# Performance work log

Measured on AMD Instinct MI355X. Metric: run time of the kernel, lower is better.

Reference implementation:

```python
import jax, jax.numpy as jnp
import numpy as np

EMBED = 256; HEADS = 8; LEVELS = 4; POINTS = 4; HID = 1024
HD = EMBED // HEADS
SHAPES = [(100, 100), (50, 50), (25, 25), (13, 13)]
STARTS = [0]
for _h, _w in SHAPES[:-1]:
    STARTS.append(STARTS[-1] + _h * _w)
TOTAL = sum(h * w for h, w in SHAPES)
BS = 2
EPS = 1e-5


def _ln(x, g, b):
    m = x.mean(-1, keepdims=True)
    v = ((x - m) ** 2).mean(-1, keepdims=True)
    return (x - m) / jnp.sqrt(v + EPS) * g + b


def _msda(query, value, ref, norm_wh, params):
    W_value, b_value, W_off, b_off, W_attn, b_attn, W_out, b_out = params
    bs, T, _ = query.shape
    v = (value @ W_value + b_value).reshape(bs, T, HEADS, HD)
    v = jnp.moveaxis(v, 2, 1)  # [bs, H, T, hd]
    off = (query @ W_off + b_off).reshape(bs, T, HEADS, LEVELS, POINTS, 2)
    aw = (query @ W_attn + b_attn).reshape(bs, T, HEADS, LEVELS * POINTS)
    aw = jax.nn.softmax(aw, axis=-1).reshape(bs, T, HEADS, LEVELS, POINTS)
    aw = jnp.moveaxis(aw, 2, 1)  # [bs, H, T, L, P]
    # sampling locations in [0,1] coords: ref + offset / (W_l, H_l)
    loc = ref[:, :, None, :, None, :] + off / norm_wh[None, None, None, :, None, :]
    loc = jnp.moveaxis(loc, 2, 1)  # [bs, H, T, L, P, 2]
    out = jnp.zeros((bs, HEADS, T, HD), query.dtype)
    for l, (Hl, Wl) in enumerate(SHAPES):
        s = STARTS[l]
        v_l = v[:, :, s:s + Hl * Wl]  # [bs, H, HW_l, hd]
        # grid_sample(align_corners=False): pixel = loc * size - 0.5
        x = loc[:, :, :, l, :, 0] * Wl - 0.5  # [bs, H, T, P]
        y = loc[:, :, :, l, :, 1] * Hl - 0.5
        x0 = jnp.floor(x); y0 = jnp.floor(y)
        wx1 = x - x0; wy1 = y - y0
        x0i = x0.astype(jnp.int32); y0i = y0.astype(jnp.int32)

        def samp(xi, yi):
            valid = (xi >= 0) & (xi < Wl) & (yi >= 0) & (yi < Hl)
            idx = jnp.clip(yi, 0, Hl - 1) * Wl + jnp.clip(xi, 0, Wl - 1)
            idx = idx.reshape(bs, HEADS, -1)
            g = jnp.take_along_axis(v_l, idx[..., None], axis=2)
            g = g.reshape(bs, HEADS, T, POINTS, HD)
            return g * valid[..., None].astype(g.dtype)

        bil = ((1 - wy1) * (1 - wx1))[..., None] * samp(x0i, y0i) \
            + ((1 - wy1) * wx1)[..., None] * samp(x0i + 1, y0i) \
            + (wy1 * (1 - wx1))[..., None] * samp(x0i, y0i + 1) \
            + (wy1 * wx1)[..., None] * samp(x0i + 1, y0i + 1)
        out = out + (bil * aw[:, :, :, l, :, None]).sum(axis=3)
    out = jnp.moveaxis(out, 1, 2).reshape(bs, T, EMBED)
    return out @ W_out + b_out


def setup_inputs() -> dict:
    key = jax.random.key(0)
    ks = jax.random.split(key, 16)
    s = 0.02
    f32 = jnp.float32
    return {
        "src": jax.random.normal(ks[0], (BS, TOTAL, EMBED), f32),
        "pos": jax.random.normal(ks[1], (BS, TOTAL, EMBED), f32),
        "reference_points": jax.random.uniform(ks[2], (BS, TOTAL, LEVELS, 2), f32),
        "spatial_shapes": jnp.array(SHAPES, jnp.int32),
        "level_start_index": jnp.array(STARTS, jnp.int32),
        "ln1_g": jnp.ones((EMBED,), f32), "ln1_b": jnp.zeros((EMBED,), f32),
        "ln2_g": jnp.ones((EMBED,), f32), "ln2_b": jnp.zeros((EMBED,), f32),
        "W_value": jax.random.normal(ks[3], (EMBED, EMBED), f32) * s,
        "b_value": jnp.zeros((EMBED,), f32),
        "W_off": jax.random.normal(ks[4], (EMBED, HEADS * LEVELS * POINTS * 2), f32) * s,
        "b_off": jax.random.normal(ks[5], (HEADS * LEVELS * POINTS * 2,), f32) * 0.5,
        "W_attn": jax.random.normal(ks[6], (EMBED, HEADS * LEVELS * POINTS), f32) * s,
        "b_attn": jnp.zeros((HEADS * LEVELS * POINTS,), f32),
        "W_out": jax.random.normal(ks[7], (EMBED, EMBED), f32) * s,
        "b_out": jnp.zeros((EMBED,), f32),
        "W_ffn1": jax.random.normal(ks[8], (EMBED, HID), f32) * s,
        "b_ffn1": jnp.zeros((HID,), f32),
        "W_ffn2": jax.random.normal(ks[9], (HID, EMBED), f32) * s,
        "b_ffn2": jnp.zeros((EMBED,), f32),
    }


def reference(src, pos, reference_points, spatial_shapes, level_start_index,
              ln1_g, ln1_b, ln2_g, ln2_b,
              W_value, b_value, W_off, b_off, W_attn, b_attn, W_out, b_out,
              W_ffn1, b_ffn1, W_ffn2, b_ffn2):
    src_n = _ln(src, ln1_g, ln1_b)
    q = src_n + pos
    # offset normalizer is (W_l, H_l)
    norm_wh = jnp.stack([spatial_shapes[:, 1], spatial_shapes[:, 0]], -1).astype(src.dtype)
    attn = _msda(q, src_n, reference_points, norm_wh,
                 (W_value, b_value, W_off, b_off, W_attn, b_attn, W_out, b_out))
    src1 = src + attn  # dropout = identity (eval)
    src_n2 = _ln(src1, ln2_g, ln2_b)
    ffn = jax.nn.relu(src_n2 @ W_ffn1 + b_ffn1) @ W_ffn2 + b_ffn2
    return src1 + ffn
```

## Files before the change

### kernel.cpp

```cpp
#include <hip/hip_runtime.h>
#include <hip/hip_bf16.h>

#define T_TOK   13294
#define BS_     2
#define M_ROWS  (BS_ * T_TOK)
#define EMBED_  256
#define HID_    1024

typedef __attribute__((ext_vector_type(8))) short short8;
typedef __attribute__((ext_vector_type(4))) float f32x4;

__device__ __forceinline__ unsigned short f2bf(float f) {
  __hip_bfloat16 h = __float2bfloat16(f);
  return *reinterpret_cast<unsigned short*>(&h);
}
__device__ __forceinline__ float bf2f(unsigned short u) {
  unsigned int x = ((unsigned int)u) << 16;
  return __uint_as_float(x);
}

__global__ __launch_bounds__(256) void transpose_all_kernel(
    const float* __restrict__ s0, const float* __restrict__ s1,
    const float* __restrict__ s2, const float* __restrict__ s3,
    const float* __restrict__ s4, const float* __restrict__ s5,
    unsigned short* __restrict__ d0, unsigned short* __restrict__ d1,
    unsigned short* __restrict__ d2, unsigned short* __restrict__ d3,
    unsigned short* __restrict__ d4, unsigned short* __restrict__ d5) {
  __shared__ float t[32][33];
  const int bid = blockIdx.x;
  const float* S; unsigned short* D; int K, N, t0;
  if      (bid <  64) { S = s0; D = d0; K = 256;  N = 256;  t0 = 0;   }
  else if (bid < 128) { S = s1; D = d1; K = 256;  N = 256;  t0 = 64;  }
  else if (bid < 160) { S = s2; D = d2; K = 256;  N = 128;  t0 = 128; }
  else if (bid < 224) { S = s3; D = d3; K = 256;  N = 256;  t0 = 160; }
  else if (bid < 480) { S = s4; D = d4; K = 256;  N = 1024; t0 = 224; }
  else                { S = s5; D = d5; K = 1024; N = 256;  t0 = 480; }
  const int tile = bid - t0;
  const int ntx = N >> 5;
  const int k0 = (tile / ntx) * 32, n0 = (tile % ntx) * 32;
  const int tx = threadIdx.x, ty = threadIdx.y;
  #pragma unroll
  for (int i = 0; i < 32; i += 8)
    t[ty + i][tx] = S[(size_t)(k0 + ty + i) * N + n0 + tx];
  __syncthreads();
  #pragma unroll
  for (int i = 0; i < 32; i += 8)
    D[(size_t)(n0 + ty + i) * K + k0 + tx] = f2bf(t[tx][ty + i]);
}

template <bool ADDPOS>
__global__ __launch_bounds__(256) void ln4_kernel(
    const float* __restrict__ x, const float* __restrict__ pos,
    const float* __restrict__ g, const float* __restrict__ bta,
    unsigned short* __restrict__ y, unsigned short* __restrict__ q) {
  const int wave = threadIdx.x >> 6, lane = threadIdx.x & 63;
  const int r = blockIdx.x * 4 + wave;
  const size_t base = (size_t)r * 256 + lane * 4;
  const float4 v = *reinterpret_cast<const float4*>(&x[base]);

  float s = v.x + v.y + v.z + v.w;
  #pragma unroll
  for (int m = 32; m; m >>= 1) s += __shfl_xor(s, m, 64);
  const float mean = s * (1.0f / 256.0f);

  const float dx = v.x - mean, dy = v.y - mean, dz = v.z - mean, dw = v.w - mean;
  float s2 = dx * dx + dy * dy + dz * dz + dw * dw;
  #pragma unroll
  for (int m = 32; m; m >>= 1) s2 += __shfl_xor(s2, m, 64);
  const float rinv = rsqrtf(s2 * (1.0f / 256.0f) + 1e-5f);

  const float4 gg = *reinterpret_cast<const float4*>(&g[lane * 4]);
  const float4 bb = *reinterpret_cast<const float4*>(&bta[lane * 4]);
  const float o0 = dx * rinv * gg.x + bb.x;
  const float o1 = dy * rinv * gg.y + bb.y;
  const float o2 = dz * rinv * gg.z + bb.z;
  const float o3 = dw * rinv * gg.w + bb.w;
  ushort4 yo; yo.x = f2bf(o0); yo.y = f2bf(o1); yo.z = f2bf(o2); yo.w = f2bf(o3);
  *reinterpret_cast<ushort4*>(&y[base]) = yo;
  if (ADDPOS) {
    const float4 pp = *reinterpret_cast<const float4*>(&pos[base]);
    ushort4 qo;
    qo.x = f2bf(o0 + pp.x); qo.y = f2bf(o1 + pp.y);
    qo.z = f2bf(o2 + pp.z); qo.w = f2bf(o3 + pp.w);
    *reinterpret_cast<ushort4*>(&q[base]) = qo;
  }
}

template <int EPI, int BN, bool OUTBF>
__device__ __forceinline__ void gemm_core(
    const unsigned short* __restrict__ A, const unsigned short* __restrict__ Wt,
    const float* __restrict__ bias, const float* __restrict__ R,
    void* __restrict__ Cv, void* __restrict__ Cv2,
    int M, int N, int K, int row0, int col0,
    unsigned short* As, unsigned short* Bs) {
  constexpr int MW = (BN == 128) ? 4 : 2;
  constexpr int NW = 4;

  const int tid = threadIdx.x;
  const int lane = tid & 63;
  const int w = tid >> 6;
  const int wrow = (BN == 128) ? (w >> 1) * 64 : w * 32;
  const int wcol = (BN == 128) ? (w & 1) * 64 : 0;

  f32x4 acc[MW][NW] = {};
  const int frow = lane & 15;
  const int fke = ((lane >> 4) ^ ((frow >> 1) & 3)) * 8;

  for (int k0 = 0; k0 < K; k0 += 32) {
    #pragma unroll
    for (int i = 0; i < 2; ++i) {
      const int chunk = i * 256 + tid;
      const int rrow = chunk >> 2;
      const int kgs = (chunk & 3) ^ ((rrow >> 1) & 3);
      int ga = row0 + rrow; if (ga >= M) ga = M - 1;
      __builtin_amdgcn_global_load_lds(
          (const __attribute__((address_space(1))) void*)(A + (size_t)ga * K + k0 + kgs * 8),
          (__attribute__((address_space(3))) void*)(As + chunk * 8), 16, 0, 0);
    }
    #pragma unroll
    for (int i = 0; i < BN / 64; ++i) {
      const int chunk = i * 256 + tid;
      const int rrow = chunk >> 2;
      const int kgs = (chunk & 3) ^ ((rrow >> 1) & 3);
      __builtin_amdgcn_global_load_lds(
          (const __attribute__((address_space(1))) void*)(Wt + (size_t)(col0 + rrow) * K + k0 + kgs * 8),
          (__attribute__((address_space(3))) void*)(Bs + chunk * 8), 16, 0, 0);
    }
    __syncthreads();

    short8 a[MW], b[NW];
    #pragma unroll
    for (int mi = 0; mi < MW; ++mi)
      a[mi] = *reinterpret_cast<const short8*>(&As[(wrow + mi * 16 + frow) * 32 + fke]);
    #pragma unroll
    for (int ni = 0; ni < NW; ++ni)
      b[ni] = *reinterpret_cast<const short8*>(&Bs[(wcol + ni * 16 + frow) * 32 + fke]);
    #pragma unroll
    for (int mi = 0; mi < MW; ++mi)
      #pragma unroll
      for (int ni = 0; ni < NW; ++ni)
        acc[mi][ni] = __builtin_amdgcn_mfma_f32_16x16x32_bf16(a[mi], b[ni], acc[mi][ni], 0, 0, 0);

    __syncthreads();
  }

  const int cl = lane & 15;
  const int rb = (lane >> 4) * 4;
  #pragma unroll
  for (int ni = 0; ni < NW; ++ni) {
    const int gc = col0 + wcol + ni * 16 + cl;
    float bv;
    if (EPI == 3) bv = (gc < 256) ? bias[gc] : R[gc - 256];
    else          bv = bias[gc];
    #pragma unroll
    for (int mi = 0; mi < MW; ++mi) {
      const int gr0 = row0 + wrow + mi * 16 + rb;
      #pragma unroll
      for (int r = 0; r < 4; ++r) {
        const int gr = gr0 + r;
        if (gr >= M) continue;
        float val = acc[mi][ni][r] + bv;
        if (EPI == 1) val = fmaxf(val, 0.f);
        if (EPI == 2) val += R[(size_t)gr * N + gc];
        if (EPI == 3) {
          if (gc < 256) ((unsigned short*)Cv )[(size_t)gr * 256 + gc]       = f2bf(val);
          else          ((unsigned short*)Cv2)[(size_t)gr * 128 + gc - 256] = f2bf(val);
        } else if (OUTBF) {
          ((unsigned short*)Cv)[(size_t)gr * N + gc] = f2bf(val);
        } else {
          ((float*)Cv)[(size_t)gr * N + gc] = val;
        }
      }
    }
  }
}

template <int EPI, int BN, bool OUTBF>
__global__ __launch_bounds__(256) void mgemm_k(
    const unsigned short* __restrict__ A, const unsigned short* __restrict__ Wt,
    const float* __restrict__ bias, const float* __restrict__ R,
    void* __restrict__ Cv, int M, int N, int K) {
  __shared__ unsigned short As[128 * 32];
  __shared__ unsigned short Bs[BN * 32];
  const int nwg = gridDim.x;
  const int bid = blockIdx.x;
  const int wgid = (bid & 7) * (nwg >> 3) + (bid >> 3);
  const int NT = N / BN;
  const int row0 = (wgid / NT) * 128;
  const int col0 = (wgid % NT) * BN;
  gemm_core<EPI, BN, OUTBF>(A, Wt, bias, R, Cv, nullptr, M, N, K, row0, col0, As, Bs);
}

__global__ __launch_bounds__(256) void proj_fused_kernel(
    const unsigned short* __restrict__ srcn, const unsigned short* __restrict__ q,
    const unsigned short* __restrict__ wt_val, const unsigned short* __restrict__ wt_offattn,
    const float* __restrict__ b_value, const float* __restrict__ b_off,
    const float* __restrict__ b_attn,
    unsigned short* __restrict__ vout, unsigned short* __restrict__ offout,
    unsigned short* __restrict__ awout, int M) {
  __shared__ unsigned short As[128 * 32];
  __shared__ unsigned short Bs[64 * 32];
  const int nwg = gridDim.x;
  const int bid = blockIdx.x;
  const int wgid = (bid & 7) * (nwg >> 3) + (bid >> 3);
  if (wgid < 832) {
    const int row0 = (wgid >> 2) * 128, col0 = (wgid & 3) * 64;
    gemm_core<0, 64, true>(srcn, wt_val, b_value, nullptr, vout, nullptr,
                           M, 256, 256, row0, col0, As, Bs);
  } else {
    const int id2 = wgid - 832;
    const int row0 = (id2 / 6) * 128, col0 = (id2 % 6) * 64;
    gemm_core<3, 64, false>(q, wt_offattn, b_off, b_attn, offout, awout,
                            M, 384, 256, row0, col0, As, Bs);
  }
}

__global__ __launch_bounds__(256) void msda_kernel(
    const unsigned short* __restrict__ v, const unsigned short* __restrict__ offb,
    const unsigned short* __restrict__ awl, const float* __restrict__ ref,
    unsigned short* __restrict__ outb) {
  const int r0 = blockIdx.x * 8;
  const int tid = threadIdx.x;

  __shared__ float s_aw[8 * 128];
  __shared__ float s_ref[64];
  __shared__ float2 s_wi[64 * 66];

  if (tid < 64) {
    int rr = r0 + (tid >> 3); if (rr >= M_ROWS) rr = M_ROWS - 1;
    s_ref[tid] = ref[(size_t)rr * 8 + (tid & 7)];
  }

  {
    const int g = tid >> 2, j = tid & 3;
    const int tok = g >> 3, h = g & 7;
    int rr = r0 + tok; if (rr >= M_ROWS) rr = M_ROWS - 1;
    const uint2 u = *reinterpret_cast<const uint2*>(&awl[(size_t)rr * 128 + h * 16 + j * 4]);
    const float l0 = bf2f((unsigned short)(u.x & 0xffff));
    const float l1 = bf2f((unsigned short)(u.x >> 16));
    const float l2 = bf2f((unsigned short)(u.y & 0xffff));
    const float l3 = bf2f((unsigned short)(u.y >> 16));
    float mx = fmaxf(fmaxf(l0, l1), fmaxf(l2, l3));
    mx = fmaxf(mx, __shfl_xor(mx, 1, 64));
    mx = fmaxf(mx, __shfl_xor(mx, 2, 64));
    const float e0 = expf(l0 - mx), e1 = expf(l1 - mx);
    const float e2 = expf(l2 - mx), e3 = expf(l3 - mx);
    float ss = e0 + e1 + e2 + e3;
    ss += __shfl_xor(ss, 1, 64);
    ss += __shfl_xor(ss, 2, 64);
    const float inv = 1.0f / ss;
    float4 w4; w4.x = e0 * inv; w4.y = e1 * inv; w4.z = e2 * inv; w4.w = e3 * inv;
    *reinterpret_cast<float4*>(&s_aw[g * 16 + j * 4]) = w4;
  }
  __syncthreads();

  const int HH[4] = {100, 50, 25, 13};
  const int WW[4] = {100, 50, 25, 13};
  const int SS[4] = {0, 10000, 12500, 13125};

  {
    const int pi0 = tid * 4;
    const int tok = pi0 >> 7, h = (pi0 >> 4) & 7;
    const int g = pi0 >> 4;
    const int pt0 = pi0 & 15;
    const int l = pt0 >> 2;
    int rr = r0 + tok; if (rr >= M_ROWS) rr = M_ROWS - 1;
    const float Wl = (float)WW[l], Hl = (float)HH[l];
    const float rx = s_ref[tok * 8 + l * 2], ry = s_ref[tok * 8 + l * 2 + 1];
    const uint4 uoff = *reinterpret_cast<const uint4*>(&offb[(size_t)rr * 256 + h * 32 + pt0 * 2]);
    const float4 aw4 = *reinterpret_cast<const float4*>(&s_aw[g * 16 + pt0]);
    const unsigned int uo[4] = {uoff.x, uoff.y, uoff.z, uoff.w};
    const float awv[4] = {aw4.x, aw4.y, aw4.z, aw4.w};
    #pragma unroll
    for (int p = 0; p < 4; ++p) {
      const float ox = bf2f((unsigned short)(uo[p] & 0xffff));
      const float oy = bf2f((unsigned short)(uo[p] >> 16));
      const float x = rx * Wl + ox - 0.5f;
      const float y = ry * Hl + oy - 0.5f;
      const float x0f = floorf(x), y0f = floorf(y);
      const int x0 = (int)x0f, y0 = (int)y0f;
      const float wx1 = x - x0f, wy1 = y - y0f;
      const float wx0 = 1.f - wx1, wy0 = 1.f - wy1;
      const float aw = awv[p];
      #pragma unroll
      for (int c = 0; c < 4; ++c) {
        const int xx = x0 + (c & 1), yy = y0 + (c >> 1);
        const bool valid = (xx >= 0) & (xx < WW[l]) & (yy >= 0) & (yy < HH[l]);
        const int xc = min(max(xx, 0), WW[l] - 1);
        const int yc = min(max(yy, 0), HH[l] - 1);
        float wgt = aw * ((c & 1) ? wx1 : wx0) * ((c >> 1) ? wy1 : wy0);
        wgt = valid ? wgt : 0.f;
        const int idxb = (SS[l] + yc * WW[l] + xc) * 512;
        s_wi[g * 66 + (pt0 + p) * 4 + c] = make_float2(wgt, __int_as_float(idxb));
      }
    }
  }
  __syncthreads();

  const int tok = tid >> 5;
  const int h = (tid >> 2) & 7;
  const int d8 = tid & 3;
  const int r = r0 + tok;
  const int rc = (r < M_ROWS) ? r : M_ROWS - 1;
  const int b = rc / T_TOK;
  const char* vb = (const char*)(v + (size_t)b * T_TOK * 256 + h * 32 + d8 * 8);
  const int e0 = (tok * 8 + h) * 66;

  float a0 = 0.f, a1 = 0.f, a2 = 0.f, a3 = 0.f;
  float a4 = 0.f, a5 = 0.f, a6 = 0.f, a7 = 0.f;
  #pragma unroll 8
  for (int j = 0; j < 64; ++j) {
    const float2 wi = s_wi[e0 + j];
    const float wgt = wi.x;
    const int idxb = __float_as_int(wi.y);
    const uint4 u = *reinterpret_cast<const uint4*>(vb + idxb);
    a0 = fmaf(wgt, bf2f((unsigned short)(u.x & 0xffff)), a0);
    a1 = fmaf(wgt, bf2f((unsigned short)(u.x >> 16)), a1);
    a2 = fmaf(wgt, bf2f((unsigned short)(u.y & 0xffff)), a2);
    a3 = fmaf(wgt, bf2f((unsigned short)(u.y >> 16)), a3);
    a4 = fmaf(wgt, bf2f((unsigned short)(u.z & 0xffff)), a4);
    a5 = fmaf(wgt, bf2f((unsigned short)(u.z >> 16)), a5);
    a6 = fmaf(wgt, bf2f((unsigned short)(u.w & 0xffff)), a6);
    a7 = fmaf(wgt, bf2f((unsigned short)(u.w >> 16)), a7);
  }
  if (r < M_ROWS) {
    uint4 o;
    o.x = ((unsigned int)f2bf(a0)) | ((unsigned int)f2bf(a1) << 16);
    o.y = ((unsigned int)f2bf(a2)) | ((unsigned int)f2bf(a3) << 16);
    o.z = ((unsigned int)f2bf(a4)) | ((unsigned int)f2bf(a5) << 16);
    o.w = ((unsigned int)f2bf(a6)) | ((unsigned int)f2bf(a7) << 16);
    *reinterpret_cast<uint4*>(&outb[(size_t)r * 256 + h * 32 + d8 * 8]) = o;
  }
}

extern "C" void kernel_launch(void* const* d_in, const int* in_sizes, int n_in,
                              void* d_out, int out_size, void* d_ws, size_t ws_size,
                              hipStream_t stream) {
  const float* src     = (const float*)d_in[0];
  const float* pos     = (const float*)d_in[1];
  const float* ref     = (const float*)d_in[2];
  const float* ln1_g   = (const float*)d_in[5];
  const float* ln1_b   = (const float*)d_in[6];
  const float* ln2_g   = (const float*)d_in[7];
  const float* ln2_b   = (const float*)d_in[8];
  const float* W_value = (const float*)d_in[9];
  const float* b_value = (const float*)d_in[10];
  const float* W_off   = (const float*)d_in[11];
  const float* b_off   = (const float*)d_in[12];
  const float* W_attn  = (const float*)d_in[13];
  const float* b_attn  = (const float*)d_in[14];
  const float* W_out   = (const float*)d_in[15];
  const float* b_out   = (const float*)d_in[16];
  const float* W_ffn1  = (const float*)d_in[17];
  const float* b_ffn1  = (const float*)d_in[18];
  const float* W_ffn2  = (const float*)d_in[19];
  const float* b_ffn2  = (const float*)d_in[20];
  float* out = (float*)d_out;

  const int M = M_ROWS;
  const size_t n256 = (size_t)M * 256;

  unsigned short* src_n_bf = (unsigned short*)d_ws;
  unsigned short* q_bf     = src_n_bf + n256;
  unsigned short* v_bf     = q_bf + n256;
  unsigned short* attn_bf  = v_bf + n256;
  unsigned short* sn2_bf   = attn_bf + n256;
  unsigned short* hid_bf   = sn2_bf + n256;
  unsigned short* offb     = hid_bf + (size_t)M * 1024;
  unsigned short* awbuf    = offb + n256;
  float* src1 = (float*)(awbuf + (size_t)M * 128);
  unsigned short* wt_val     = (unsigned short*)(src1 + n256);
  unsigned short* wt_offattn = wt_val + 256 * 256;
  unsigned short* wt_out     = wt_offattn + 384 * 256;
  unsigned short* wt_ffn1    = wt_out + 256 * 256;
  unsigned short* wt_ffn2    = wt_ffn1 + 1024 * 256;

  transpose_all_kernel<<<736, dim3(32, 8), 0, stream>>>(
      W_value, W_off, W_attn, W_out, W_ffn1, W_ffn2,
      wt_val, wt_offattn, wt_offattn + 256 * 256, wt_out, wt_ffn1, wt_ffn2);

  ln4_kernel<true><<<M / 4, 256, 0, stream>>>(src, pos, ln1_g, ln1_b, src_n_bf, q_bf);

  proj_fused_kernel<<<2080, 256, 0, stream>>>(
      src_n_bf, q_bf, wt_val, wt_offattn, b_value, b_off, b_attn,
      v_bf, offb, awbuf, M);

  msda_kernel<<<(M + 7) / 8, 256, 0, stream>>>(v_bf, offb, awbuf, ref, attn_bf);

  mgemm_k<2, 64, false><<<832, 256, 0, stream>>>(attn_bf, wt_out, b_out, src,
                                                 src1, M, 256, 256);

  ln4_kernel<false><<<M / 4, 256, 0, stream>>>(src1, nullptr, ln2_g, ln2_b, sn2_bf, nullptr);

  mgemm_k<1, 128, true ><<<1664, 256, 0, stream>>>(sn2_bf, wt_ffn1, b_ffn1, nullptr,
                                                   hid_bf, M, 1024, 256);
  mgemm_k<2, 64, false><<<832, 256, 0, stream>>>(hid_bf, wt_ffn2, b_ffn2, src1,
                                                 out, M, 256, 1024);
}
```

Measured before the change: 209.8 us.

## Give each wavefront its own 64x64 GEMM tile and drop block barriers

Restructures every GEMM so each of the four wavefronts in a block owns an independent 64x64 output tile with a private LDS slice. Block-wide __syncthreads are replaced by per-wave s_waitcnt, which removes cross-wave barrier stalls. MFMA operands are swapped so each lane holds four consecutive columns, allowing vectorized float4/ushort4 bias loads and output stores. In exchange, each wave loads its own A and B tiles with no sharing between waves, which raises global/L2 traffic per output element, and the per-wave LDS write-then-read now depends only on wave-local wait counts.

Measured after the change: 201.9 us. -3.8%, faster.

```diff
diff --git a/kernel.cpp b/kernel.cpp
--- a/kernel.cpp
+++ b/kernel.cpp
@@ -86,30 +86,24 @@
   }
 }
 
-template <int EPI, int BN, bool OUTBF>
-__device__ __forceinline__ void gemm_core(
+template <int EPI, bool OUTBF>
+__device__ __forceinline__ void wgemm_core(
     const unsigned short* __restrict__ A, const unsigned short* __restrict__ Wt,
     const float* __restrict__ bias, const float* __restrict__ R,
     void* __restrict__ Cv, void* __restrict__ Cv2,
-    int M, int N, int K, int row0, int col0,
-    unsigned short* As, unsigned short* Bs) {
-  constexpr int MW = (BN == 128) ? 4 : 2;
-  constexpr int NW = 4;
-
-  const int tid = threadIdx.x;
-  const int lane = tid & 63;
-  const int w = tid >> 6;
-  const int wrow = (BN == 128) ? (w >> 1) * 64 : w * 32;
-  const int wcol = (BN == 128) ? (w & 1) * 64 : 0;
-
-  f32x4 acc[MW][NW] = {};
+    int M, int N, int K, int row0, int col0, unsigned short* lds) {
+  const int lane = threadIdx.x & 63;
+  unsigned short* As = lds;
+  unsigned short* Bs = lds + 64 * 32;
+
+  f32x4 acc[4][4] = {};
   const int frow = lane & 15;
   const int fke = ((lane >> 4) ^ ((frow >> 1) & 3)) * 8;
 
   for (int k0 = 0; k0 < K; k0 += 32) {
     #pragma unroll
-    for (int i = 0; i < 2; ++i) {
-      const int chunk = i * 256 + tid;
+    for (int i = 0; i < 4; ++i) {
+      const int chunk = i * 64 + lane;
       const int rrow = chunk >> 2;
       const int kgs = (chunk & 3) ^ ((rrow >> 1) & 3);
       int ga = row0 + rrow; if (ga >= M) ga = M - 1;
@@ -118,100 +112,113 @@
           (__attribute__((address_space(3))) void*)(As + chunk * 8), 16, 0, 0);
     }
     #pragma unroll
-    for (int i = 0; i < BN / 64; ++i) {
-      const int chunk = i * 256 + tid;
+    for (int i = 0; i < 4; ++i) {
+      const int chunk = i * 64 + lane;
       const int rrow = chunk >> 2;
       const int kgs = (chunk & 3) ^ ((rrow >> 1) & 3);
       __builtin_amdgcn_global_load_lds(
           (const __attribute__((address_space(1))) void*)(Wt + (size_t)(col0 + rrow) * K + k0 + kgs * 8),
           (__attribute__((address_space(3))) void*)(Bs + chunk * 8), 16, 0, 0);
     }
-    __syncthreads();
-
-    short8 a[MW], b[NW];
-    #pragma unroll
-    for (int mi = 0; mi < MW; ++mi)
-      a[mi] = *reinterpret_cast<const short8*>(&As[(wrow + mi * 16 + frow) * 32 + fke]);
-    #pragma unroll
-    for (int ni = 0; ni < NW; ++ni)
-      b[ni] = *reinterpret_cast<const short8*>(&Bs[(wcol + ni * 16 + frow) * 32 + fke]);
-    #pragma unroll
-    for (int mi = 0; mi < MW; ++mi)
+    asm volatile("s_waitcnt vmcnt(0)" ::: "memory");
+
+    short8 a[4], b[4];
+    #pragma unroll
+    for (int mi = 0; mi < 4; ++mi)
+      a[mi] = *reinterpret_cast<const short8*>(&As[(mi * 16 + frow) * 32 + fke]);
+    #pragma unroll
+    for (int ni = 0; ni < 4; ++ni)
+      b[ni] = *reinterpret_cast<const short8*>(&Bs[(ni * 16 + frow) * 32 + fke]);
+    #pragma unroll
+    for (int mi = 0; mi < 4; ++mi)
       #pragma unroll
-      for (int ni = 0; ni < NW; ++ni)
-        acc[mi][ni] = __builtin_amdgcn_mfma_f32_16x16x32_bf16(a[mi], b[ni], acc[mi][ni], 0, 0, 0);
-
-    __syncthreads();
-  }
-
-  const int cl = lane & 15;
-  const int rb = (lane >> 4) * 4;
+      for (int ni = 0; ni < 4; ++ni)
+        acc[mi][ni] = __builtin_amdgcn_mfma_f32_16x16x32_bf16(b[ni], a[mi], acc[mi][ni], 0, 0, 0);
+    asm volatile("s_waitcnt lgkmcnt(0)" ::: "memory");
+  }
+
+  const int lr = lane & 15;
+  const int cb = (lane >> 4) * 4;
   #pragma unroll
-  for (int ni = 0; ni < NW; ++ni) {
-    const int gc = col0 + wcol + ni * 16 + cl;
-    float bv;
-    if (EPI == 3) bv = (gc < 256) ? bias[gc] : R[gc - 256];
-    else          bv = bias[gc];
-    #pragma unroll
-    for (int mi = 0; mi < MW; ++mi) {
-      const int gr0 = row0 + wrow + mi * 16 + rb;
-      #pragma unroll
-      for (int r = 0; r < 4; ++r) {
-        const int gr = gr0 + r;
-        if (gr >= M) continue;
-        float val = acc[mi][ni][r] + bv;
-        if (EPI == 1) val = fmaxf(val, 0.f);
-        if (EPI == 2) val += R[(size_t)gr * N + gc];
+  for (int mi = 0; mi < 4; ++mi) {
+    const int grow = row0 + mi * 16 + lr;
+    if (grow >= M) continue;
+    #pragma unroll
+    for (int ni = 0; ni < 4; ++ni) {
+      const int gcol = col0 + ni * 16 + cb;
+      float4 b4;
+      if (EPI == 3) b4 = (gcol < 256) ? *reinterpret_cast<const float4*>(&bias[gcol])
+                                      : *reinterpret_cast<const float4*>(&R[gcol - 256]);
+      else          b4 = *reinterpret_cast<const float4*>(&bias[gcol]);
+      float v0 = acc[mi][ni][0] + b4.x;
+      float v1 = acc[mi][ni][1] + b4.y;
+      float v2 = acc[mi][ni][2] + b4.z;
+      float v3 = acc[mi][ni][3] + b4.w;
+      if (EPI == 1) {
+        v0 = fmaxf(v0, 0.f); v1 = fmaxf(v1, 0.f);
+        v2 = fmaxf(v2, 0.f); v3 = fmaxf(v3, 0.f);
+      }
+      if (EPI == 2) {
+        const float4 r4 = *reinterpret_cast<const float4*>(&R[(size_t)grow * N + gcol]);
+        v0 += r4.x; v1 += r4.y; v2 += r4.z; v3 += r4.w;
+        float4 o; o.x = v0; o.y = v1; o.z = v2; o.w = v3;
+        *reinterpret_cast<float4*>(&((float*)Cv)[(size_t)grow * N + gcol]) = o;
+      } else {
+        ushort4 o;
+        o.x = f2bf(v0); o.y = f2bf(v1); o.z = f2bf(v2); o.w = f2bf(v3);
         if (EPI == 3) {
-          if (gc < 256) ((unsigned short*)Cv )[(size_t)gr * 256 + gc]       = f2bf(val);
-          else          ((unsigned short*)Cv2)[(size_t)gr * 128 + gc - 256] = f2bf(val);
-        } else if (OUTBF) {
-          ((unsigned short*)Cv)[(size_t)gr * N + gc] = f2bf(val);
+          if (gcol < 256)
+            *reinterpret_cast<ushort4*>(&((unsigned short*)Cv )[(size_t)grow * 256 + gcol]) = o;
+          else
+            *reinterpret_cast<ushort4*>(&((unsigned short*)Cv2)[(size_t)grow * 128 + gcol - 256]) = o;
         } else {
-          ((float*)Cv)[(size_t)gr * N + gc] = val;
+          *reinterpret_cast<ushort4*>(&((unsigned short*)Cv)[(size_t)grow * N + gcol]) = o;
         }
       }
     }
   }
 }
 
-template <int EPI, int BN, bool OUTBF>
-__global__ __launch_bounds__(256) void mgemm_k(
+template <int EPI, bool OUTBF>
+__global__ __launch_bounds__(256) void wgemm_k(
     const unsigned short* __restrict__ A, const unsigned short* __restrict__ Wt,
     const float* __restrict__ bias, const float* __restrict__ R,
     void* __restrict__ Cv, int M, int N, int K) {
-  __shared__ unsigned short As[128 * 32];
-  __shared__ unsigned short Bs[BN * 32];
+  __shared__ unsigned short lds[4 * 4096];
+  const int w = threadIdx.x >> 6;
   const int nwg = gridDim.x;
   const int bid = blockIdx.x;
   const int wgid = (bid & 7) * (nwg >> 3) + (bid >> 3);
-  const int NT = N / BN;
-  const int row0 = (wgid / NT) * 128;
-  const int col0 = (wgid % NT) * BN;
-  gemm_core<EPI, BN, OUTBF>(A, Wt, bias, R, Cv, nullptr, M, N, K, row0, col0, As, Bs);
-}
-
-__global__ __launch_bounds__(256) void proj_fused_kernel(
+  const int tile = wgid * 4 + w;
+  const int CT = N >> 6;
+  const int row0 = (tile / CT) * 64;
+  const int col0 = (tile % CT) * 64;
+  wgemm_core<EPI, OUTBF>(A, Wt, bias, R, Cv, nullptr, M, N, K, row0, col0,
+                         lds + w * 4096);
+}
+
+__global__ __launch_bounds__(256) void wproj_fused(
     const unsigned short* __restrict__ srcn, const unsigned short* __restrict__ q,
     const unsigned short* __restrict__ wt_val, const unsigned short* __restrict__ wt_offattn,
     const float* __restrict__ b_value, const float* __restrict__ b_off,
     const float* __restrict__ b_attn,
     unsigned short* __restrict__ vout, unsigned short* __restrict__ offout,
     unsigned short* __restrict__ awout, int M) {
-  __shared__ unsigned short As[128 * 32];
-  __shared__ unsigned short Bs[64 * 32];
+  __shared__ unsigned short lds[4 * 4096];
+  const int w = threadIdx.x >> 6;
   const int nwg = gridDim.x;
   const int bid = blockIdx.x;
   const int wgid = (bid & 7) * (nwg >> 3) + (bid >> 3);
-  if (wgid < 832) {
-    const int row0 = (wgid >> 2) * 128, col0 = (wgid & 3) * 64;
-    gemm_core<0, 64, true>(srcn, wt_val, b_value, nullptr, vout, nullptr,
-                           M, 256, 256, row0, col0, As, Bs);
+  const int tile = wgid * 4 + w;
+  if (tile < 1664) {
+    const int row0 = (tile >> 2) * 64, col0 = (tile & 3) * 64;
+    wgemm_core<0, true>(srcn, wt_val, b_value, nullptr, vout, nullptr,
+                        M, 256, 256, row0, col0, lds + w * 4096);
   } else {
-    const int id2 = wgid - 832;
-    const int row0 = (id2 / 6) * 128, col0 = (id2 % 6) * 64;
-    gemm_core<3, 64, false>(q, wt_offattn, b_off, b_attn, offout, awout,
-                            M, 384, 256, row0, col0, As, Bs);
+    const int t2 = tile - 1664;
+    const int row0 = (t2 / 6) * 64, col0 = (t2 % 6) * 64;
+    wgemm_core<3, false>(q, wt_offattn, b_off, b_attn, offout, awout,
+                         M, 384, 256, row0, col0, lds + w * 4096);
   }
 }
 
@@ -381,19 +388,19 @@
 
   ln4_kernel<true><<<M / 4, 256, 0, stream>>>(src, pos, ln1_g, ln1_b, src_n_bf, q_bf);
 
-  proj_fused_kernel<<<2080, 256, 0, stream>>>(
+  wproj_fused<<<1040, 256, 0, stream>>>(
       src_n_bf, q_bf, wt_val, wt_offattn, b_value, b_off, b_attn,
       v_bf, offb, awbuf, M);
 
   msda_kernel<<<(M + 7) / 8, 256, 0, stream>>>(v_bf, offb, awbuf, ref, attn_bf);
 
-  mgemm_k<2, 64, false><<<832, 256, 0, stream>>>(attn_bf, wt_out, b_out, src,
-                                                 src1, M, 256, 256);
+  wgemm_k<2, false><<<416, 256, 0, stream>>>(attn_bf, wt_out, b_out, src,
+                                             src1, M, 256, 256);
 
   ln4_kernel<false><<<M / 4, 256, 0, stream>>>(src1, nullptr, ln2_g, ln2_b, sn2_bf, nullptr);
 
-  mgemm_k<1, 128, true ><<<1664, 256, 0, stream>>>(sn2_bf, wt_ffn1, b_ffn1, nullptr,
-                                                   hid_bf, M, 1024, 256);
-  mgemm_k<2, 64, false><<<832, 256, 0, stream>>>(hid_bf, wt_ffn2, b_ffn2, src1,
-                                                 out, M, 256, 1024);
-}
+  wgemm_k<1, true ><<<1664, 256, 0, stream>>>(sn2_bf, wt_ffn1, b_ffn1, nullptr,
+                                              hid_bf, M, 1024, 256);
+  wgemm_k<2, false><<<416, 256, 0, stream>>>(hid_bf, wt_ffn2, b_ffn2, src1,
+                                             out, M, 256, 1024);
+}
```
